# Kernel tuning notes

Hardware: AMD Instinct MI355X
Metric: run time of the kernel (lower is better)

## Reference

```python
import jax, jax.numpy as jnp
import numpy as np

R, N_X, N_MONTE = 8192, 32, 64


def setup_inputs() -> dict:
    key = jax.random.key(0)
    ks = jax.random.split(key, 6)
    # SPD per-step Hessian blocks (recog_x_prec_tilde is PSD by construction in the model)
    B = jax.random.normal(ks[0], (R, N_X, N_X), dtype=jnp.float32)
    x_hessian_diags = jnp.einsum('rij,rkj->rik', B, B) / N_X + jnp.eye(N_X, dtype=jnp.float32)
    x_grads = jax.random.normal(ks[1], (R, 1, N_X), dtype=jnp.float32)
    x_trans_mat = 0.5 * jnp.eye(N_X, dtype=jnp.float32) + 0.1 * jax.random.normal(ks[2], (N_X, N_X), dtype=jnp.float32)
    A = jax.random.normal(ks[3], (N_X, N_X), dtype=jnp.float32)
    x_trans_prec = A @ A.T / N_X + jnp.eye(N_X, dtype=jnp.float32)
    Bi = jax.random.normal(ks[4], (N_X, N_X), dtype=jnp.float32)
    x_init_prec = Bi @ Bi.T / N_X + jnp.eye(N_X, dtype=jnp.float32)
    epsx = jax.random.normal(ks[5], (R, N_MONTE, N_X), dtype=jnp.float32)
    return dict(x_hessian_diags=x_hessian_diags, x_grads=x_grads, x_trans_mat=x_trans_mat,
                x_trans_prec=x_trans_prec, x_init_prec=x_init_prec, epsx=epsx)


def _cholesky_update(x_hessian_diags, x_grads, x_trans_mat, x_trans_prec, x_init_prec, epsx):
    Rn, n_monte, n_x = epsx.shape
    solve = jax.scipy.linalg.solve_triangular
    MtP = x_trans_mat @ x_trans_prec          # [n_x, n_x]
    MtPMt = MtP @ x_trans_mat.T               # [n_x, n_x]
    # last step has no transition term (m=0), matching ms = [1,...,1,0]
    ms = jnp.concatenate([jnp.ones((Rn - 1,), jnp.float32), jnp.zeros((1,), jnp.float32)])

    def fwd(carry, elem):
        P, C, u = carry                       # predicted prec, off-diag chol, u
        H, g, m = elem
        L = jnp.linalg.cholesky(P + H + m * MtPMt)          # [n_x, n_x] lower
        u = solve(L, (g - u @ C.T).T, lower=True).T         # [1, n_x]
        C = solve(L, -MtP, lower=True).T                    # [n_x, n_x]
        P = x_trans_prec - C @ C.T
        return (P, C, u), (L, C, u)

    z = jnp.zeros((n_x, n_x), jnp.float32)
    init = (x_init_prec, z, jnp.zeros((1, n_x), jnp.float32))
    _, (Ls, Cs, us) = jax.lax.scan(fwd, init, (x_hessian_diags, x_grads, ms))

    gs = jnp.concatenate([us, epsx], axis=1)  # [R, 1+n_monte, n_x]

    def bwd(vw, elem):
        L, C, g = elem
        vw = solve(L.T, (g - vw @ C).T, lower=False).T      # [1+n_monte, n_x]
        return vw, vw

    _, vws = jax.lax.scan(bwd, jnp.zeros((n_monte + 1, n_x), jnp.float32),
                          (Ls, Cs, gs), reverse=True)
    vs, ws = vws[:, :1], vws[:, 1:]           # posterior mean part, sample part
    return Ls, Cs, vs, ws


def reference(x_hessian_diags, x_grads, x_trans_mat, x_trans_prec, x_init_prec, epsx):
    _, _, vs, ws = _cholesky_update(x_hessian_diags, x_grads, x_trans_mat,
                                    x_trans_prec, x_init_prec, epsx)
    # x_tilde = vs_tilde + ws_tilde as used downstream in _compute_eta_loss_2
    return vs + ws                            # [R, n_monte, n_x]
```

## Files before the change

kernel.cpp:

```cpp
#include <hip/hip_runtime.h>
#include <stdint.h>

#define RTOT 8192
#define BFWD 4
#define WFWD 12
#define BBWD 8
#define WBWD 16
#define LSTR 36

typedef unsigned short u16;
typedef __attribute__((ext_vector_type(4))) float f32x4;
typedef __attribute__((ext_vector_type(8))) unsigned short u16x8;

__device__ __forceinline__ float bf2f(u16 u) { return __uint_as_float(((uint32_t)u) << 16); }
__device__ __forceinline__ float rdlane(float v, int l) {
  return __int_as_float(__builtin_amdgcn_readlane(__float_as_int(v), l));
}

__device__ __forceinline__ void load8(const void* p, size_t off, bool bf, float* o) {
  if (bf) {
    u16x8 v = *(const u16x8*)((const u16*)p + off);
    #pragma unroll
    for (int e = 0; e < 8; ++e) o[e] = bf2f(v[e]);
  } else {
    f32x4 a = *(const f32x4*)((const float*)p + off);
    f32x4 b = *(const f32x4*)((const float*)p + off + 4);
    o[0]=a[0]; o[1]=a[1]; o[2]=a[2]; o[3]=a[3];
    o[4]=b[0]; o[5]=b[1]; o[6]=b[2]; o[7]=b[3];
  }
}
__device__ __forceinline__ float load1(const void* p, size_t off, bool bf) {
  return bf ? bf2f(((const u16*)p)[off]) : ((const float*)p)[off];
}

__global__ void detect_kernel(const void* Wptr, int* flag) {
  if (threadIdx.x == 0) {
    const u16* w = (const u16*)Wptr;
    int ok = 1;
    const int pi[4] = {0, 0, 1, 2};
    const int pj[4] = {1, 2, 2, 3};
    #pragma unroll
    for (int p = 0; p < 4; ++p)
      ok &= (w[pi[p]*32 + pj[p]] == w[pj[p]*32 + pi[p]]) ? 1 : 0;
    *flag = ok;
  }
}

__global__ __launch_bounds__(64, 2) void fwd_kernel(
    const void* __restrict__ Hg, const void* __restrict__ Gg,
    const void* __restrict__ Mg, const void* __restrict__ Wg,
    const void* __restrict__ Ig, int s0, const int* __restrict__ flag,
    float* __restrict__ gLinv, float* __restrict__ gCt, float* __restrict__ gU)
{
  __shared__ __align__(16) float ldsCt[32*LSTR];
  __shared__ __align__(16) float ldsLinv[32*LSTR];
  __shared__ float ldsU[32];

  const bool bf = (*flag != 0);
  const int lane = threadIdx.x & 63;
  const int il = lane & 31;
  const bool lo = (lane < 32);
  const int hoff = (lane >> 5) * 16;

  float wrow[32], mrow[32];
  #pragma unroll
  for (int c = 0; c < 4; ++c) {
    float wt[8], mt[8];
    load8(Wg, il*32 + c*8, bf, wt);
    load8(Mg, il*32 + c*8, bf, mt);
    #pragma unroll
    for (int e = 0; e < 8; ++e) {
      wrow[c*8+e] = wt[e]; mrow[c*8+e] = mt[e];
      ldsCt[il*LSTR + c*8+e] = mt[e];
    }
  }
  __syncthreads();

  #pragma unroll 4
  for (int m = 0; m < 32; ++m) {
    float acc = 0.0f;
    #pragma unroll
    for (int c = 0; c < 8; ++c) {
      f32x4 q = *(const f32x4*)&ldsCt[m*LSTR + c*4];
      acc = fmaf(q[0], wrow[c*4+0], acc); acc = fmaf(q[1], wrow[c*4+1], acc);
      acc = fmaf(q[2], wrow[c*4+2], acc); acc = fmaf(q[3], wrow[c*4+3], acc);
    }
    ldsLinv[m*LSTR + il] = acc;
  }
  __syncthreads();
  #pragma unroll 4
  for (int m = 0; m < 32; ++m) {
    float acc = 0.0f;
    #pragma unroll
    for (int c = 0; c < 8; ++c) {
      f32x4 q = *(const f32x4*)&ldsLinv[m*LSTR + c*4];
      acc = fmaf(q[0], mrow[c*4+0], acc); acc = fmaf(q[1], mrow[c*4+1], acc);
      acc = fmaf(q[2], mrow[c*4+2], acc); acc = fmaf(q[3], mrow[c*4+3], acc);
    }
    ldsCt[m*LSTR + il] = acc;
  }
  __syncthreads();

  float mtpcol[32];
  #pragma unroll
  for (int t = 0; t < 32; ++t) mtpcol[t] = ldsLinv[t*LSTR + il];
  float k0h[16];
  #pragma unroll
  for (int c = 0; c < 16; ++c) {
    float a = wrow[c]      + ldsCt[il*LSTR + c];
    float b = wrow[c + 16] + ldsCt[il*LSTR + 16 + c];
    k0h[c] = lo ? a : b;
  }
  __syncthreads();

  #pragma unroll
  for (int k = 0; k < 32; ++k) ldsCt[il*LSTR + k] = 0.0f;
  if (lo) ldsU[il] = 0.0f;
  __syncthreads();

  const int r0 = s0 + blockIdx.x * BFWD;
  const int rw0 = (r0 >= WFWD) ? (r0 - WFWD) : 0;
  const int rend = r0 + BFWD;

  float hcur[16];
  #pragma unroll
  for (int c = 0; c < 2; ++c)
    load8(Hg, (size_t)rw0*1024 + il*32 + hoff + c*8, bf, &hcur[c*8]);
  float gv = load1(Gg, (size_t)rw0*32 + il, bf);

  for (int r = rw0; r < rend; ++r) {
    int rn = (r + 1 < RTOT) ? (r + 1) : r;
    float hnext[16];
    #pragma unroll
    for (int c = 0; c < 2; ++c)
      load8(Hg, (size_t)rn*1024 + il*32 + hoff + c*8, bf, &hnext[c*8]);
    float gvn = load1(Gg, (size_t)rn*32 + il, bf);

    float sv[16];
    if (r == 0) {
      #pragma unroll
      for (int c = 0; c < 2; ++c) {
        float it[8], wt[8];
        load8(Ig, il*32 + hoff + c*8, bf, it);
        load8(Wg, il*32 + hoff + c*8, bf, wt);
        #pragma unroll
        for (int e = 0; e < 8; ++e)
          sv[c*8+e] = hcur[c*8+e] + it[e] + (k0h[c*8+e] - wt[e]);
      }
    } else if (r == RTOT - 1) {
      #pragma unroll
      for (int c = 0; c < 2; ++c) {
        float wt[8];
        load8(Wg, il*32 + hoff + c*8, bf, wt);
        #pragma unroll
        for (int e = 0; e < 8; ++e) sv[c*8+e] = hcur[c*8+e] + wt[e];
      }
    } else {
      #pragma unroll
      for (int k = 0; k < 16; ++k) sv[k] = hcur[k] + k0h[k];
    }

    float y = gv;
    #pragma unroll 4
    for (int m = 0; m < 32; ++m) {
      float cm = ldsCt[m*LSTR + il];
      y = fmaf(ldsU[m], cm, y);
      #pragma unroll
      for (int c = 0; c < 4; ++c) {
        f32x4 q = *(const f32x4*)&ldsCt[m*LSTR + hoff + c*4];
        sv[c*4+0] = fmaf(-cm, q[0], sv[c*4+0]);
        sv[c*4+1] = fmaf(-cm, q[1], sv[c*4+1]);
        sv[c*4+2] = fmaf(-cm, q[2], sv[c*4+2]);
        sv[c*4+3] = fmaf(-cm, q[3], sv[c*4+3]);
      }
    }

    float v[32];
    #pragma unroll
    for (int c = 0; c < 16; ++c) {
      float o = __shfl_xor(sv[c], 32, 64);
      v[c]      = lo ? sv[c] : mtpcol[c];
      v[c + 16] = lo ? o     : mtpcol[c + 16];
    }

    float un = 0.0f;
    float yr = y;
    if (r < r0) {
      #pragma unroll
      for (int j = 0; j < 32; ++j) {
        float dj = fmaxf(rdlane(v[j], j), 1e-12f);
        float rs = __builtin_amdgcn_rsqf(dj);
        float a = v[j] * rs;
        v[j] = a;
        float uj = rdlane(yr, j) * rs;
        yr = fmaf(-a, uj, yr);
        if (il == j) un = uj;
        #pragma unroll
        for (int k = j + 1; k < 32; ++k) {
          float bk = rdlane(v[j], k);
          v[k] = fmaf(-a, bk, v[k]);
        }
      }
    } else {
      float w[32];
      #pragma unroll
      for (int i = 0; i < 32; ++i) w[i] = (lo && il == i) ? 1.0f : 0.0f;
      #pragma unroll
      for (int j = 0; j < 32; ++j) {
        float dj = fmaxf(rdlane(v[j], j), 1e-12f);
        float rs = __builtin_amdgcn_rsqf(dj);
        float a = v[j] * rs;
        v[j] = a;
        float b = w[j] * rs;
        w[j] = b;
        float uj = rdlane(yr, j) * rs;
        yr = fmaf(-a, uj, yr);
        if (il == j) un = uj;
        #pragma unroll
        for (int k = j + 1; k < 32; ++k) {
          float bk = rdlane(v[j], k);
          v[k] = fmaf(-a, bk, v[k]);
          w[k] = fmaf(-b, bk, w[k]);
        }
      }
      if (lo) {
        #pragma unroll
        for (int i = 0; i < 32; ++i) ldsLinv[i*LSTR + il] = w[i];
      }
    }

    if (!lo) {
      #pragma unroll
      for (int m = 0; m < 32; ++m) ldsCt[m*LSTR + il] = v[m];
    } else {
      ldsU[il] = un;
    }

    if (r >= r0) {
      __syncthreads();
      size_t ro = (size_t)(r - s0);
      #pragma unroll
      for (int c = 0; c < 4; ++c) {
        int f = lane*16 + c*4;
        int mm = f >> 5, kk = f & 31;
        *(f32x4*)&gLinv[ro*1024 + f] = *(const f32x4*)&ldsLinv[mm*LSTR + kk];
        *(f32x4*)&gCt [ro*1024 + f] = *(const f32x4*)&ldsCt [mm*LSTR + kk];
      }
      if (lo) gU[ro*32 + il] = un;
    }

    #pragma unroll
    for (int e = 0; e < 16; ++e) hcur[e] = hnext[e];
    gv = gvn;
  }
}

__global__ __launch_bounds__(256, 2) void mid_kernel(
    const void* __restrict__ Eg, const int* __restrict__ flag,
    float* __restrict__ gLinv, float* __restrict__ gCt,
    const float* __restrict__ gU, float* __restrict__ gY2, int s0)
{
  __shared__ __align__(16) float Li[32*LSTR];
  __shared__ __align__(16) float Ct_[32*LSTR];
  __shared__ float Ut[32];
  __shared__ float Y0l[32];

  const bool bf = (*flag != 0);
  const int t = threadIdx.x;
  const size_t ro = blockIdx.x;
  const size_t r = (size_t)s0 + ro;

  {
    int mm = t >> 3, kk = (t & 7) * 4;
    *(f32x4*)&Li[mm*LSTR + kk]  = *(const f32x4*)&gLinv[ro*1024 + t*4];
    *(f32x4*)&Ct_[mm*LSTR + kk] = *(const f32x4*)&gCt [ro*1024 + t*4];
    if (t < 32) Ut[t] = gU[ro*32 + t];
  }
  __syncthreads();

  if (t < 32) {
    float a = 0.0f;
    #pragma unroll
    for (int k = 0; k < 32; ++k) a = fmaf(Ut[k], Li[k*LSTR + t], a);
    Y0l[t] = a;
  }
  __syncthreads();

  {
    int s = t >> 2, oct = t & 3;
    float er[32];
    #pragma unroll
    for (int c = 0; c < 4; ++c) load8(Eg, (r*64 + (size_t)s)*32 + c*8, bf, &er[c*8]);
    float a0=0,a1=0,a2=0,a3=0,a4=0,a5=0,a6=0,a7=0;
    #pragma unroll 4
    for (int k = 0; k < 32; ++k) {
      f32x4 b  = *(const f32x4*)&Li[k*LSTR + oct*8];
      f32x4 b2 = *(const f32x4*)&Li[k*LSTR + oct*8 + 4];
      float ek = er[k];
      a0=fmaf(ek,b[0],a0);  a1=fmaf(ek,b[1],a1);
      a2=fmaf(ek,b[2],a2);  a3=fmaf(ek,b[3],a3);
      a4=fmaf(ek,b2[0],a4); a5=fmaf(ek,b2[1],a5);
      a6=fmaf(ek,b2[2],a6); a7=fmaf(ek,b2[3],a7);
    }
    f32x4 y0a = *(const f32x4*)&Y0l[oct*8];
    f32x4 y0b = *(const f32x4*)&Y0l[oct*8 + 4];
    float* dst = (s < 32) ? (gLinv + ro*1024 + (size_t)s*32)
                          : (gY2  + ro*1024 + (size_t)(s-32)*32);
    f32x4 va = {a0+y0a[0], a1+y0a[1], a2+y0a[2], a3+y0a[3]};
    f32x4 vb = {a4+y0b[0], a5+y0b[1], a6+y0b[2], a7+y0b[3]};
    *(f32x4*)&dst[oct*8] = va;
    *(f32x4*)&dst[oct*8 + 4] = vb;
  }

  {
    int m = t >> 3, jo = t & 7;
    float d0=0,d1=0,d2=0,d3=0;
    #pragma unroll 4
    for (int k = 0; k < 32; ++k) {
      float cv = Ct_[k*LSTR + m];
      f32x4 b = *(const f32x4*)&Li[k*LSTR + jo*4];
      d0=fmaf(cv,b[0],d0); d1=fmaf(cv,b[1],d1);
      d2=fmaf(cv,b[2],d2); d3=fmaf(cv,b[3],d3);
    }
    f32x4 dv = {d0,d1,d2,d3};
    *(f32x4*)&gCt[ro*1024 + (size_t)m*32 + jo*4] = dv;
  }
}

__global__ __launch_bounds__(64, 1) void bwd_kernel(
    const float* __restrict__ gD,
    const float* __restrict__ gY1,
    const float* __restrict__ gY2,
    float* __restrict__ outg, int s0)
{
  const int l = threadIdx.x & 63;
  const int lr = l & 31;
  const int dco = (l >> 5) * 16;
  const int r0 = s0 + blockIdx.x * BBWD;
  int re = r0 + BBWD - 1 + WBWD; if (re > RTOT - 1) re = RTOT - 1;

  const float* Yb = (l < 32) ? gY1 : gY2;

  float vwr[32];
  #pragma unroll
  for (int k = 0; k < 32; ++k) vwr[k] = 0.0f;

  const int reo = re - s0;
  f32x4 Dc[4], Yc[8];
  #pragma unroll
  for (int c = 0; c < 4; ++c)
    Dc[c] = *(const f32x4*)&gD[(size_t)reo*1024 + (size_t)lr*32 + dco + c*4];
  #pragma unroll
  for (int c = 0; c < 8; ++c)
    Yc[c] = *(const f32x4*)&Yb[(size_t)reo*1024 + (size_t)lr*32 + c*4];

  for (int r = re; r >= r0; --r) {
    const int ro = r - s0;

    f32x4 Dn[4], Yn[8];
    if (r > r0) {
      #pragma unroll
      for (int c = 0; c < 4; ++c)
        Dn[c] = *(const f32x4*)&gD[(size_t)(ro-1)*1024 + (size_t)lr*32 + dco + c*4];
      #pragma unroll
      for (int c = 0; c < 8; ++c)
        Yn[c] = *(const f32x4*)&Yb[(size_t)(ro-1)*1024 + (size_t)lr*32 + c*4];
    }

    float nv[32];
    #pragma unroll
    for (int j = 0; j < 32; ++j) {
      float acc = Yc[j >> 2][j & 3];
      const int cidx = j & 15;
      const int sadd = (j >> 4) << 5;
      #pragma unroll
      for (int k = 0; k < 32; ++k) {
        float dkj = rdlane(Dc[cidx >> 2][cidx & 3], k + sadd);
        acc = fmaf(vwr[k], dkj, acc);
      }
      nv[j] = acc;
    }

    if (r < r0 + BBWD) {
      float* dst = outg + ((size_t)r * 64 + (size_t)l) * 32;
      #pragma unroll
      for (int c = 0; c < 8; ++c) {
        f32x4 o = { nv[c*4+0], nv[c*4+1], nv[c*4+2], nv[c*4+3] };
        *(f32x4*)&dst[c*4] = o;
      }
    }

    #pragma unroll
    for (int k = 0; k < 32; ++k) vwr[k] = nv[k];
    if (r > r0) {
      #pragma unroll
      for (int c = 0; c < 4; ++c) Dc[c] = Dn[c];
      #pragma unroll
      for (int c = 0; c < 8; ++c) Yc[c] = Yn[c];
    }
  }
}

extern "C" void kernel_launch(void* const* d_in, const int* in_sizes, int n_in,
                              void* d_out, int out_size, void* d_ws, size_t ws_size,
                              hipStream_t stream) {
  (void)in_sizes; (void)n_in; (void)out_size;
  const void* H = d_in[0];
  const void* G = d_in[1];
  const void* M = d_in[2];
  const void* W = d_in[3];
  const void* I = d_in[4];
  const void* E = d_in[5];
  float* out = (float*)d_out;

  int* flag = (int*)d_ws;
  float* ws0 = (float*)((char*)d_ws + 256);
  size_t avail = (ws_size > 256) ? (ws_size - 256) : 0;

  int nseg = 64;
  for (int cand = 1; cand <= 64; cand <<= 1) {
    size_t nrext = (size_t)(RTOT / cand) + WBWD;
    if (nrext * 12416 <= avail) { nseg = cand; break; }
  }
  const int segrows = RTOT / nseg;
  const size_t nrext_max = (size_t)segrows + WBWD;

  float* gLinv = ws0;
  float* gCt  = ws0 + nrext_max * 1024;
  float* gU   = ws0 + nrext_max * 2048;
  float* gY2  = ws0 + nrext_max * 2080;

  detect_kernel<<<1, 64, 0, stream>>>(W, flag);

  for (int s = 0; s < nseg; ++s) {
    int s0 = s * segrows;
    int s1ext = s0 + segrows + WBWD; if (s1ext > RTOT) s1ext = RTOT;
    int nr = s1ext - s0;
    int nfb = (nr + BFWD - 1) / BFWD;
    fwd_kernel<<<nfb, 64, 0, stream>>>(H, G, M, W, I, s0, flag, gLinv, gCt, gU);
    mid_kernel<<<nr, 256, 0, stream>>>(E, flag, gLinv, gCt, gU, gY2, s0);
    bwd_kernel<<<segrows / BBWD, 64, 0, stream>>>(gCt, gLinv, gY2, out, s0);
  }
}
```

Measured before the change: 483.6 us.

## Split backward sweep across blocks by sample rows and use LDS for D

```diff
diff --git a/kernel.cpp b/kernel.cpp
--- a/kernel.cpp
+++ b/kernel.cpp
@@ -4,7 +4,7 @@
 #define RTOT 8192
 #define BFWD 4
 #define WFWD 12
-#define BBWD 8
+#define BBWD 16
 #define WBWD 16
 #define LSTR 36
 
@@ -327,76 +327,92 @@
   }
 }
 
-__global__ __launch_bounds__(64, 1) void bwd_kernel(
+__global__ __launch_bounds__(64, 2) void bwd_kernel(
     const float* __restrict__ gD,
     const float* __restrict__ gY1,
     const float* __restrict__ gY2,
-    float* __restrict__ outg, int s0)
+    float* __restrict__ outg, int s0, int nrb)
 {
+  __shared__ __align__(16) float vw[16*LSTR];
+  __shared__ __align__(16) float Dl[32*LSTR];
+
   const int l = threadIdx.x & 63;
-  const int lr = l & 31;
-  const int dco = (l >> 5) * 16;
-  const int r0 = s0 + blockIdx.x * BBWD;
+  const int prl = l >> 3;
+  const int o = l & 7;
+  const int rb = blockIdx.x % nrb;
+  const int q = blockIdx.x / nrb;
+  const int pr = q*8 + prl;
+
+  const int r0 = s0 + rb * BBWD;
   int re = r0 + BBWD - 1 + WBWD; if (re > RTOT - 1) re = RTOT - 1;
 
-  const float* Yb = (l < 32) ? gY1 : gY2;
-
-  float vwr[32];
-  #pragma unroll
-  for (int k = 0; k < 32; ++k) vwr[k] = 0.0f;
+  {
+    f32x4 z = {0,0,0,0};
+    *(f32x4*)&vw[prl*LSTR + o*4] = z;
+    *(f32x4*)&vw[(8+prl)*LSTR + o*4] = z;
+  }
 
   const int reo = re - s0;
-  f32x4 Dc[4], Yc[8];
+  f32x4 Dc[4], yA, yB;
   #pragma unroll
   for (int c = 0; c < 4; ++c)
-    Dc[c] = *(const f32x4*)&gD[(size_t)reo*1024 + (size_t)lr*32 + dco + c*4];
-  #pragma unroll
-  for (int c = 0; c < 8; ++c)
-    Yc[c] = *(const f32x4*)&Yb[(size_t)reo*1024 + (size_t)lr*32 + c*4];
+    Dc[c] = *(const f32x4*)&gD[(size_t)reo*1024 + l*16 + c*4];
+  yA = *(const f32x4*)&gY1[(size_t)reo*1024 + pr*32 + o*4];
+  yB = *(const f32x4*)&gY2[(size_t)reo*1024 + pr*32 + o*4];
 
   for (int r = re; r >= r0; --r) {
     const int ro = r - s0;
 
-    f32x4 Dn[4], Yn[8];
+    #pragma unroll
+    for (int c = 0; c < 4; ++c) {
+      int off = l*16 + c*4;
+      *(f32x4*)&Dl[(off >> 5)*LSTR + (off & 31)] = Dc[c];
+    }
+
+    f32x4 Dn[4], ynA, ynB;
     if (r > r0) {
       #pragma unroll
       for (int c = 0; c < 4; ++c)
-        Dn[c] = *(const f32x4*)&gD[(size_t)(ro-1)*1024 + (size_t)lr*32 + dco + c*4];
-      #pragma unroll
-      for (int c = 0; c < 8; ++c)
-        Yn[c] = *(const f32x4*)&Yb[(size_t)(ro-1)*1024 + (size_t)lr*32 + c*4];
-    }
-
-    float nv[32];
-    #pragma unroll
-    for (int j = 0; j < 32; ++j) {
-      float acc = Yc[j >> 2][j & 3];
-      const int cidx = j & 15;
-      const int sadd = (j >> 4) << 5;
-      #pragma unroll
-      for (int k = 0; k < 32; ++k) {
-        float dkj = rdlane(Dc[cidx >> 2][cidx & 3], k + sadd);
-        acc = fmaf(vwr[k], dkj, acc);
-      }
-      nv[j] = acc;
-    }
+        Dn[c] = *(const f32x4*)&gD[(size_t)(ro-1)*1024 + l*16 + c*4];
+      ynA = *(const f32x4*)&gY1[(size_t)(ro-1)*1024 + pr*32 + o*4];
+      ynB = *(const f32x4*)&gY2[(size_t)(ro-1)*1024 + pr*32 + o*4];
+    }
+
+    float vA[32], vB[32];
+    #pragma unroll
+    for (int c = 0; c < 8; ++c) {
+      f32x4 qa = *(const f32x4*)&vw[prl*LSTR + c*4];
+      f32x4 qb = *(const f32x4*)&vw[(8+prl)*LSTR + c*4];
+      vA[c*4+0]=qa[0]; vA[c*4+1]=qa[1]; vA[c*4+2]=qa[2]; vA[c*4+3]=qa[3];
+      vB[c*4+0]=qb[0]; vB[c*4+1]=qb[1]; vB[c*4+2]=qb[2]; vB[c*4+3]=qb[3];
+    }
+
+    float a0=yA[0],a1=yA[1],a2=yA[2],a3=yA[3];
+    float b0=yB[0],b1=yB[1],b2=yB[2],b3=yB[3];
+    #pragma unroll 4
+    for (int k = 0; k < 32; ++k) {
+      f32x4 d = *(const f32x4*)&Dl[k*LSTR + o*4];
+      float xa = vA[k], xb = vB[k];
+      a0=fmaf(xa,d[0],a0); a1=fmaf(xa,d[1],a1);
+      a2=fmaf(xa,d[2],a2); a3=fmaf(xa,d[3],a3);
+      b0=fmaf(xb,d[0],b0); b1=fmaf(xb,d[1],b1);
+      b2=fmaf(xb,d[2],b2); b3=fmaf(xb,d[3],b3);
+    }
+    f32x4 va = {a0,a1,a2,a3}, vb = {b0,b1,b2,b3};
+    *(f32x4*)&vw[prl*LSTR + o*4] = va;
+    *(f32x4*)&vw[(8+prl)*LSTR + o*4] = vb;
 
     if (r < r0 + BBWD) {
-      float* dst = outg + ((size_t)r * 64 + (size_t)l) * 32;
-      #pragma unroll
-      for (int c = 0; c < 8; ++c) {
-        f32x4 o = { nv[c*4+0], nv[c*4+1], nv[c*4+2], nv[c*4+3] };
-        *(f32x4*)&dst[c*4] = o;
-      }
-    }
-
-    #pragma unroll
-    for (int k = 0; k < 32; ++k) vwr[k] = nv[k];
+      float* dstA = outg + ((size_t)r*64 + (size_t)pr)*32 + o*4;
+      float* dstB = outg + ((size_t)r*64 + (size_t)(pr+32))*32 + o*4;
+      *(f32x4*)dstA = va;
+      *(f32x4*)dstB = vb;
+    }
+
     if (r > r0) {
       #pragma unroll
       for (int c = 0; c < 4; ++c) Dc[c] = Dn[c];
-      #pragma unroll
-      for (int c = 0; c < 8; ++c) Yc[c] = Yn[c];
+      yA = ynA; yB = ynB;
     }
   }
 }
@@ -437,8 +453,9 @@
     int s1ext = s0 + segrows + WBWD; if (s1ext > RTOT) s1ext = RTOT;
     int nr = s1ext - s0;
     int nfb = (nr + BFWD - 1) / BFWD;
+    int nrb = segrows / BBWD;
     fwd_kernel<<<nfb, 64, 0, stream>>>(H, G, M, W, I, s0, flag, gLinv, gCt, gU);
     mid_kernel<<<nr, 256, 0, stream>>>(E, flag, gLinv, gCt, gU, gY2, s0);
-    bwd_kernel<<<segrows / BBWD, 64, 0, stream>>>(gCt, gLinv, gY2, out, s0);
-  }
-}
+    bwd_kernel<<<nrb * 4, 64, 0, stream>>>(gCt, gLinv, gY2, out, s0, nrb);
+  }
+}
```

Measured after the change: 398.0 us. 17.7% less time.
